# Performance work log

Measured on AMD Instinct MI355X. Metric: run time of the kernel, lower is better.

The kernel has to match this reference:

```python
import jax, jax.numpy as jnp
import numpy as np

ROI_POOLING_SIZE = 7
CROP = ROI_POOLING_SIZE * 2  # before_pooling_size = 14


def _crop_and_resize(img, boxes, crop):
    """tf.image.crop_and_resize (bilinear, extrapolation_value=0) for a single image.

    img:   [H, W, C]
    boxes: [N, 4] normalized [y1, x1, y2, x2]
    returns [N, crop, crop, C]
    """
    H, W, C = img.shape
    y1, x1, y2, x2 = boxes[:, 0], boxes[:, 1], boxes[:, 2], boxes[:, 3]
    idx = jnp.arange(crop, dtype=img.dtype)  # crop > 1 branch of TF semantics
    # sample coordinates in source-pixel space: [N, crop]
    ys = y1[:, None] * (H - 1) + idx[None, :] * ((y2 - y1) * (H - 1) / (crop - 1))[:, None]
    xs = x1[:, None] * (W - 1) + idx[None, :] * ((x2 - x1) * (W - 1) / (crop - 1))[:, None]

    y0f = jnp.floor(ys)
    x0f = jnp.floor(xs)
    ly = ys - y0f  # bilinear fractional weights [N, crop]
    lx = xs - x0f

    y0 = jnp.clip(y0f.astype(jnp.int32), 0, H - 1)
    y1i = jnp.clip(y0 + 1, 0, H - 1)
    x0 = jnp.clip(x0f.astype(jnp.int32), 0, W - 1)
    x1i = jnp.clip(x0 + 1, 0, W - 1)

    # out-of-image samples get extrapolation_value = 0
    vy = (ys >= 0) & (ys <= H - 1)  # [N, crop]
    vx = (xs >= 0) & (xs <= W - 1)

    # irregular per-box bilinear gather: val[n,i,j,c] = img[y[n,i], x[n,j], c]
    def g(yi, xi):
        return img[yi[:, :, None], xi[:, None, :]]  # [N, crop, crop, C]

    v00 = g(y0, x0)
    v01 = g(y0, x1i)
    v10 = g(y1i, x0)
    v11 = g(y1i, x1i)

    lxb = lx[:, None, :, None]
    lyb = ly[:, :, None, None]
    top = v00 + (v01 - v00) * lxb
    bot = v10 + (v11 - v10) * lxb
    val = top + (bot - top) * lyb

    valid = (vy[:, :, None] & vx[:, None, :])[..., None]
    return jnp.where(valid, val, jnp.zeros((), dtype=img.dtype))


def reference(feature_maps, proposals, image_shape):
    # proposals are pixel-space [x1, y1, x2, y2]; normalize to [y1/h, x1/w, y2/h, x2/w]
    h = image_shape[0].astype(jnp.float32)
    w = image_shape[1].astype(jnp.float32)
    boxes = jnp.stack(
        [proposals[:, 1] / h, proposals[:, 0] / w, proposals[:, 3] / h, proposals[:, 2] / w],
        axis=1,
    )
    crops = _crop_and_resize(feature_maps[0], boxes, CROP)  # [N, 14, 14, C]
    N, Hc, Wc, C = crops.shape
    # MaxPooling2D(pool=2, stride=2, padding='same'); 14 is even so no padding needed
    pooled = crops.reshape(N, Hc // 2, 2, Wc // 2, 2, C).max(axis=(2, 4))
    return pooled  # [N, 7, 7, C]


def setup_inputs() -> dict:
    key = jax.random.key(0)
    k1, k2, k3, k4, k5 = jax.random.split(key, 5)
    H_img, W_img = 800, 1216
    N = 2000
    feature_maps = jax.random.normal(k1, (1, 200, 304, 256), dtype=jnp.float32)
    # realistic boxes in image pixel coords [x1, y1, x2, y2]
    x1 = jax.random.uniform(k2, (N,), minval=0.0, maxval=0.75 * W_img)
    y1 = jax.random.uniform(k3, (N,), minval=0.0, maxval=0.75 * H_img)
    bw = jax.random.uniform(k4, (N,), minval=16.0, maxval=0.25 * W_img)
    bh = jax.random.uniform(k5, (N,), minval=16.0, maxval=0.25 * H_img)
    proposals = jnp.stack([x1, y1, jnp.minimum(x1 + bw, W_img - 1.0), jnp.minimum(y1 + bh, H_img - 1.0)], axis=1).astype(jnp.float32)
    image_shape = jnp.array([H_img, W_img], dtype=jnp.int32)
    return {"feature_maps": feature_maps, "proposals": proposals, "image_shape": image_shape}
```

## Files before the change

### kernel.cpp

```cpp
#include <hip/hip_runtime.h>
#include <math.h>

#define H_FM 200
#define W_FM 304
#define C_FM 256
#define NPIX (H_FM * W_FM)
#define CROP 14
#define PH 7
#define NPOS 49
#define SLABS 16
#define SLAB_C 16
#define SLAB_ELEMS (NPIX * SLAB_C)

typedef float floatx4 __attribute__((ext_vector_type(4)));

__global__ __launch_bounds__(256) void repack_kernel(
    const float* __restrict__ fm,
    float*       __restrict__ slabbed)
{
    const int idx = blockIdx.x * 256 + threadIdx.x;
    const int p   = idx >> 6;
    const int c4  = idx & 63;
    const int s   = c4 >> 2;
    const int cq  = c4 & 3;
    const float4 v = *(const float4*)(fm + (size_t)idx * 4);
    *(float4*)(slabbed + (size_t)s * SLAB_ELEMS + (size_t)p * SLAB_C + cq * 4) = v;
}

template <bool SLABBED>
__global__ __launch_bounds__(256) void roi_pool_slab_kernel(
    const float* __restrict__ fmbase,
    const float* __restrict__ proposals,
    const int*   __restrict__ image_shape,
    float*       __restrict__ out,
    int N)
{
    const int bid   = blockIdx.x;
    const int xcd   = bid & 7;
    const int j     = bid >> 3;
    const int phase = j / N;
    const int n     = j - phase * N;
    const int slab  = phase * 8 + xcd;
    const int c0    = slab * SLAB_C;

    const int tid  = threadIdx.x;
    const int pgrp = tid >> 4;
    const int sub  = tid & 15;
    const int s    = sub >> 2;
    const int a    = s >> 1;
    const int b    = s & 1;
    const int q    = sub & 3;

    const float himg = (float)image_shape[0];
    const float wimg = (float)image_shape[1];

    const float bx1 = proposals[n * 4 + 0] / wimg;
    const float by1 = proposals[n * 4 + 1] / himg;
    const float bx2 = proposals[n * 4 + 2] / wimg;
    const float by2 = proposals[n * 4 + 3] / himg;

    const float Hm1 = (float)(H_FM - 1);
    const float Wm1 = (float)(W_FM - 1);

    const float ybase = by1 * Hm1;
    const float xbase = bx1 * Wm1;
    const float ystep = (by2 - by1) * Hm1 / (float)(CROP - 1);
    const float xstep = (bx2 - bx1) * Wm1 / (float)(CROP - 1);

    const float* fmq = SLABBED
        ? fmbase + (size_t)slab * SLAB_ELEMS + q * 4
        : fmbase + c0 + q * 4;
    const int PIX_STRIDE = SLABBED ? SLAB_C : C_FM;

    #pragma unroll
    for (int it = 0; it < 4; ++it) {
        const int p = it * 16 + pgrp;
        const bool active = (p < NPOS);

        float vx_ = 0.0f, vy_ = 0.0f, vz_ = 0.0f, vw_ = 0.0f;

        if (active) {
            const int py = p / PH;
            const int px = p - py * PH;

            const float ysv = ybase + (float)(2 * py + a) * ystep;
            const float xsv = xbase + (float)(2 * px + b) * xstep;

            const float y0f = floorf(ysv);
            const float ly  = ysv - y0f;
            int y0 = (int)y0f;
            y0 = min(max(y0, 0), H_FM - 1);
            const int y1c = min(y0 + 1, H_FM - 1);

            const float x0f = floorf(xsv);
            const float lx  = xsv - x0f;
            int x0 = (int)x0f;
            x0 = min(max(x0, 0), W_FM - 1);
            const int x1c = min(x0 + 1, W_FM - 1);

            const bool valid = (ysv >= 0.0f) && (ysv <= Hm1) &&
                               (xsv >= 0.0f) && (xsv <= Wm1);

            if (valid) {
                const float4 v00 = *(const float4*)(fmq + (size_t)(y0  * W_FM + x0 ) * PIX_STRIDE);
                const float4 v01 = *(const float4*)(fmq + (size_t)(y0  * W_FM + x1c) * PIX_STRIDE);
                const float4 v10 = *(const float4*)(fmq + (size_t)(y1c * W_FM + x0 ) * PIX_STRIDE);
                const float4 v11 = *(const float4*)(fmq + (size_t)(y1c * W_FM + x1c) * PIX_STRIDE);

                float tx, ty, tz, tw, bx, by, bz, bw;
                tx = v00.x + (v01.x - v00.x) * lx;
                ty = v00.y + (v01.y - v00.y) * lx;
                tz = v00.z + (v01.z - v00.z) * lx;
                tw = v00.w + (v01.w - v00.w) * lx;
                bx = v10.x + (v11.x - v10.x) * lx;
                by = v10.y + (v11.y - v10.y) * lx;
                bz = v10.z + (v11.z - v10.z) * lx;
                bw = v10.w + (v11.w - v10.w) * lx;
                vx_ = tx + (bx - tx) * ly;
                vy_ = ty + (by - ty) * ly;
                vz_ = tz + (bz - tz) * ly;
                vw_ = tw + (bw - tw) * ly;
            }
        }

        vx_ = fmaxf(vx_, __shfl_xor(vx_, 4));
        vy_ = fmaxf(vy_, __shfl_xor(vy_, 4));
        vz_ = fmaxf(vz_, __shfl_xor(vz_, 4));
        vw_ = fmaxf(vw_, __shfl_xor(vw_, 4));
        vx_ = fmaxf(vx_, __shfl_xor(vx_, 8));
        vy_ = fmaxf(vy_, __shfl_xor(vy_, 8));
        vz_ = fmaxf(vz_, __shfl_xor(vz_, 8));
        vw_ = fmaxf(vw_, __shfl_xor(vw_, 8));

        if (active && s == 0) {
            floatx4 v;
            v.x = vx_; v.y = vy_; v.z = vz_; v.w = vw_;
            floatx4* outp = (floatx4*)(out + ((size_t)n * NPOS + p) * C_FM + c0 + q * 4);
            __builtin_nontemporal_store(v, outp);
        }
    }
}

extern "C" void kernel_launch(void* const* d_in, const int* in_sizes, int n_in,
                              void* d_out, int out_size, void* d_ws, size_t ws_size,
                              hipStream_t stream) {
    const float* fm        = (const float*)d_in[0];
    const float* proposals = (const float*)d_in[1];
    const int*   imshape   = (const int*)d_in[2];
    float* out = (float*)d_out;

    const int N = in_sizes[1] / 4;
    const size_t needed = (size_t)SLABS * SLAB_ELEMS * sizeof(float);

    if (ws_size >= needed) {
        repack_kernel<<<NPIX / 4, 256, 0, stream>>>(fm, (float*)d_ws);
        roi_pool_slab_kernel<true><<<SLABS * N, 256, 0, stream>>>(
            (const float*)d_ws, proposals, imshape, out, N);
    } else {
        roi_pool_slab_kernel<false><<<SLABS * N, 256, 0, stream>>>(
            fm, proposals, imshape, out, N);
    }
}
```

Measured before the change: 220.1 us.

## Replace slab repack with one block per ROI using shared sample tables

Drops the channel-slab repack kernel and the 16-blocks-per-ROI XCD-aware grid. Each ROI now runs in a single block: 196 threads first write bilinear offsets and premultiplied weights into shared memory, then each wave covers all 256 channels (one float4 per lane) for a range of pooled positions and takes the 2x2 max in registers instead of through shuffles. This removes the repack traffic and the repeated per-thread coordinate math, and gives each gather a full contiguous 1 KB pixel row. In exchange it loses the slab layout's L2 locality per XCD and runs with fewer, longer blocks, with uneven position counts across the four waves.

```diff
diff --git a/kernel.cpp b/kernel.cpp
--- a/kernel.cpp
+++ b/kernel.cpp
@@ -4,160 +4,144 @@
 #define H_FM 200
 #define W_FM 304
 #define C_FM 256
-#define NPIX (H_FM * W_FM)
+#define PIXB (C_FM * 4)
 #define CROP 14
 #define PH 7
 #define NPOS 49
-#define SLABS 16
-#define SLAB_C 16
-#define SLAB_ELEMS (NPIX * SLAB_C)
+#define NSAMP (NPOS * 4)
 
 typedef float floatx4 __attribute__((ext_vector_type(4)));
 
-__global__ __launch_bounds__(256) void repack_kernel(
+__global__ __launch_bounds__(256) void roi_pool_kernel(
     const float* __restrict__ fm,
-    float*       __restrict__ slabbed)
-{
-    const int idx = blockIdx.x * 256 + threadIdx.x;
-    const int p   = idx >> 6;
-    const int c4  = idx & 63;
-    const int s   = c4 >> 2;
-    const int cq  = c4 & 3;
-    const float4 v = *(const float4*)(fm + (size_t)idx * 4);
-    *(float4*)(slabbed + (size_t)s * SLAB_ELEMS + (size_t)p * SLAB_C + cq * 4) = v;
-}
-
-template <bool SLABBED>
-__global__ __launch_bounds__(256) void roi_pool_slab_kernel(
-    const float* __restrict__ fmbase,
     const float* __restrict__ proposals,
     const int*   __restrict__ image_shape,
     float*       __restrict__ out,
     int N)
 {
-    const int bid   = blockIdx.x;
-    const int xcd   = bid & 7;
-    const int j     = bid >> 3;
-    const int phase = j / N;
-    const int n     = j - phase * N;
-    const int slab  = phase * 8 + xcd;
-    const int c0    = slab * SLAB_C;
+    __shared__ uint4  gO[NSAMP];
+    __shared__ float4 gW[NSAMP];
 
-    const int tid  = threadIdx.x;
-    const int pgrp = tid >> 4;
-    const int sub  = tid & 15;
-    const int s    = sub >> 2;
-    const int a    = s >> 1;
-    const int b    = s & 1;
-    const int q    = sub & 3;
+    const int n   = blockIdx.x;
+    const int tid = threadIdx.x;
 
-    const float himg = (float)image_shape[0];
-    const float wimg = (float)image_shape[1];
+    if (tid < NSAMP) {
+        const int s  = tid & 3;
+        const int p  = tid >> 2;
+        const int py = p / PH;
+        const int px = p - py * PH;
+        const int a  = s >> 1;
+        const int b  = s & 1;
 
-    const float bx1 = proposals[n * 4 + 0] / wimg;
-    const float by1 = proposals[n * 4 + 1] / himg;
-    const float bx2 = proposals[n * 4 + 2] / wimg;
-    const float by2 = proposals[n * 4 + 3] / himg;
+        const float himg = (float)image_shape[0];
+        const float wimg = (float)image_shape[1];
 
-    const float Hm1 = (float)(H_FM - 1);
-    const float Wm1 = (float)(W_FM - 1);
+        const float bx1 = proposals[n * 4 + 0] / wimg;
+        const float by1 = proposals[n * 4 + 1] / himg;
+        const float bx2 = proposals[n * 4 + 2] / wimg;
+        const float by2 = proposals[n * 4 + 3] / himg;
 
-    const float ybase = by1 * Hm1;
-    const float xbase = bx1 * Wm1;
-    const float ystep = (by2 - by1) * Hm1 / (float)(CROP - 1);
-    const float xstep = (bx2 - bx1) * Wm1 / (float)(CROP - 1);
+        const float Hm1 = (float)(H_FM - 1);
+        const float Wm1 = (float)(W_FM - 1);
 
-    const float* fmq = SLABBED
-        ? fmbase + (size_t)slab * SLAB_ELEMS + q * 4
-        : fmbase + c0 + q * 4;
-    const int PIX_STRIDE = SLABBED ? SLAB_C : C_FM;
+        const float ystep = (by2 - by1) * Hm1 / (float)(CROP - 1);
+        const float xstep = (bx2 - bx1) * Wm1 / (float)(CROP - 1);
+        const float ys = by1 * Hm1 + (float)(2 * py + a) * ystep;
+        const float xs = bx1 * Wm1 + (float)(2 * px + b) * xstep;
 
-    #pragma unroll
-    for (int it = 0; it < 4; ++it) {
-        const int p = it * 16 + pgrp;
-        const bool active = (p < NPOS);
+        const float y0f = floorf(ys);
+        const float x0f = floorf(xs);
+        const float ly  = ys - y0f;
+        const float lx  = xs - x0f;
 
-        float vx_ = 0.0f, vy_ = 0.0f, vz_ = 0.0f, vw_ = 0.0f;
+        int y0 = min(max((int)y0f, 0), H_FM - 1);
+        int x0 = min(max((int)x0f, 0), W_FM - 1);
+        const int dy = min(y0 + 1, H_FM - 1) - y0;
+        const int dx = min(x0 + 1, W_FM - 1) - x0;
 
-        if (active) {
-            const int py = p / PH;
-            const int px = p - py * PH;
+        const bool valid = (ys >= 0.0f) && (ys <= Hm1) &&
+                           (xs >= 0.0f) && (xs <= Wm1);
+        const float vf   = valid ? 1.0f : 0.0f;
+        const float omlx = 1.0f - lx;
+        const float omly = 1.0f - ly;
 
-            const float ysv = ybase + (float)(2 * py + a) * ystep;
-            const float xsv = xbase + (float)(2 * px + b) * xstep;
+        float4 w;
+        w.x = omlx * omly * vf;
+        w.y = lx   * omly * vf;
+        w.z = omlx * ly   * vf;
+        w.w = lx   * ly   * vf;
 
-            const float y0f = floorf(ysv);
-            const float ly  = ysv - y0f;
-            int y0 = (int)y0f;
-            y0 = min(max(y0, 0), H_FM - 1);
-            const int y1c = min(y0 + 1, H_FM - 1);
+        uint4 o;
+        o.x = (uint32_t)(y0 * W_FM + x0) * PIXB;
+        o.y = (uint32_t)dx * PIXB;
+        o.z = (uint32_t)(dy * W_FM) * PIXB;
+        o.w = 0u;
 
-            const float x0f = floorf(xsv);
-            const float lx  = xsv - x0f;
-            int x0 = (int)x0f;
-            x0 = min(max(x0, 0), W_FM - 1);
-            const int x1c = min(x0 + 1, W_FM - 1);
+        gO[tid] = o;
+        gW[tid] = w;
+    }
+    __syncthreads();
 
-            const bool valid = (ysv >= 0.0f) && (ysv <= Hm1) &&
-                               (xsv >= 0.0f) && (xsv <= Wm1);
+    const int wave = tid >> 6;
+    const int lane = tid & 63;
+    const uint32_t laneB = (uint32_t)lane * 16u;
+    const char* fmB  = (const char*)fm;
+    char*       outB = (char*)out + (size_t)n * (NPOS * PIXB);
 
-            if (valid) {
-                const float4 v00 = *(const float4*)(fmq + (size_t)(y0  * W_FM + x0 ) * PIX_STRIDE);
-                const float4 v01 = *(const float4*)(fmq + (size_t)(y0  * W_FM + x1c) * PIX_STRIDE);
-                const float4 v10 = *(const float4*)(fmq + (size_t)(y1c * W_FM + x0 ) * PIX_STRIDE);
-                const float4 v11 = *(const float4*)(fmq + (size_t)(y1c * W_FM + x1c) * PIX_STRIDE);
+    const int pbeg = (wave * NPOS) >> 2;
+    const int pend = ((wave + 1) * NPOS) >> 2;
 
-                float tx, ty, tz, tw, bx, by, bz, bw;
-                tx = v00.x + (v01.x - v00.x) * lx;
-                ty = v00.y + (v01.y - v00.y) * lx;
-                tz = v00.z + (v01.z - v00.z) * lx;
-                tw = v00.w + (v01.w - v00.w) * lx;
-                bx = v10.x + (v11.x - v10.x) * lx;
-                by = v10.y + (v11.y - v10.y) * lx;
-                bz = v10.z + (v11.z - v10.z) * lx;
-                bw = v10.w + (v11.w - v10.w) * lx;
-                vx_ = tx + (bx - tx) * ly;
-                vy_ = ty + (by - ty) * ly;
-                vz_ = tz + (bz - tz) * ly;
-                vw_ = tw + (bw - tw) * ly;
+    for (int p = pbeg; p < pend; ++p) {
+        float4 m;
+        #pragma unroll
+        for (int s = 0; s < 4; ++s) {
+            const uint4  o = gO[p * 4 + s];
+            const float4 w = gW[p * 4 + s];
+
+            const uint32_t o00 = o.x + laneB;
+            const uint32_t o01 = o00 + o.y;
+            const uint32_t o10 = o00 + o.z;
+            const uint32_t o11 = o10 + o.y;
+
+            const float4 t00 = *(const float4*)(fmB + o00);
+            const float4 t01 = *(const float4*)(fmB + o01);
+            const float4 t10 = *(const float4*)(fmB + o10);
+            const float4 t11 = *(const float4*)(fmB + o11);
+
+            float4 v;
+            v.x = fmaf(t00.x, w.x, fmaf(t01.x, w.y, fmaf(t10.x, w.z, t11.x * w.w)));
+            v.y = fmaf(t00.y, w.x, fmaf(t01.y, w.y, fmaf(t10.y, w.z, t11.y * w.w)));
+            v.z = fmaf(t00.z, w.x, fmaf(t01.z, w.y, fmaf(t10.z, w.z, t11.z * w.w)));
+            v.w = fmaf(t00.w, w.x, fmaf(t01.w, w.y, fmaf(t10.w, w.z, t11.w * w.w)));
+
+            if (s == 0) {
+                m = v;
+            } else {
+                m.x = fmaxf(m.x, v.x);
+                m.y = fmaxf(m.y, v.y);
+                m.z = fmaxf(m.z, v.z);
+                m.w = fmaxf(m.w, v.w);
             }
         }
 
-        vx_ = fmaxf(vx_, __shfl_xor(vx_, 4));
-        vy_ = fmaxf(vy_, __shfl_xor(vy_, 4));
-        vz_ = fmaxf(vz_, __shfl_xor(vz_, 4));
-        vw_ = fmaxf(vw_, __shfl_xor(vw_, 4));
-        vx_ = fmaxf(vx_, __shfl_xor(vx_, 8));
-        vy_ = fmaxf(vy_, __shfl_xor(vy_, 8));
-        vz_ = fmaxf(vz_, __shfl_xor(vz_, 8));
-        vw_ = fmaxf(vw_, __shfl_xor(vw_, 8));
-
-        if (active && s == 0) {
-            floatx4 v;
-            v.x = vx_; v.y = vy_; v.z = vz_; v.w = vw_;
-            floatx4* outp = (floatx4*)(out + ((size_t)n * NPOS + p) * C_FM + c0 + q * 4);
-            __builtin_nontemporal_store(v, outp);
-        }
+        floatx4 mv;
+        mv.x = m.x; mv.y = m.y; mv.z = m.z; mv.w = m.w;
+        __builtin_nontemporal_store(mv,
+            (floatx4*)(outB + (uint32_t)p * PIXB + laneB));
     }
 }
 
 extern "C" void kernel_launch(void* const* d_in, const int* in_sizes, int n_in,
                               void* d_out, int out_size, void* d_ws, size_t ws_size,
                               hipStream_t stream) {
+    (void)d_ws; (void)ws_size; (void)n_in; (void)out_size;
+
     const float* fm        = (const float*)d_in[0];
     const float* proposals = (const float*)d_in[1];
     const int*   imshape   = (const int*)d_in[2];
     float* out = (float*)d_out;
 
     const int N = in_sizes[1] / 4;
-    const size_t needed = (size_t)SLABS * SLAB_ELEMS * sizeof(float);
 
-    if (ws_size >= needed) {
-        repack_kernel<<<NPIX / 4, 256, 0, stream>>>(fm, (float*)d_ws);
-        roi_pool_slab_kernel<true><<<SLABS * N, 256, 0, stream>>>(
-            (const float*)d_ws, proposals, imshape, out, N);
-    } else {
-        roi_pool_slab_kernel<false><<<SLABS * N, 256, 0, stream>>>(
-            fm, proposals, imshape, out, N);
-    }
+    roi_pool_kernel<<<N, 256, 0, stream>>>(fm, proposals, imshape, out, N);
 }
```

Result: slower. 317.5 us (+44.2%).
